# Performance work log

Hardware: AMD Instinct MI355X
Metric: run time of the kernel (lower is better)

## Reference

```python
import jax, jax.numpy as jnp
import numpy as np

B, S, D, H = 16, 1024, 768, 12
HD = D // H  # head_dim = 64


def setup_inputs() -> dict:
    key = jax.random.key(0)
    k1, k2, k3 = jax.random.split(key, 3)
    x = jax.random.normal(k1, (B, S, D), dtype=jnp.float32)
    # torch Linear default init ~ U(-1/sqrt(in), 1/sqrt(in)); use small normal for stability
    W_qkv = jax.random.normal(k2, (D, 3 * D), dtype=jnp.float32) * 0.02
    b_qkv = jnp.zeros((3 * D,), dtype=jnp.float32)
    W_out = jax.random.normal(k3, (D, D), dtype=jnp.float32) * 0.02
    b_out = jnp.zeros((D,), dtype=jnp.float32)
    return {"x": x, "W_qkv": W_qkv, "b_qkv": b_qkv, "W_out": W_out, "b_out": b_out, "mode": 0}


def reference(x, W_qkv, b_qkv, W_out, b_out, mode):
    # x: [B, S, D]; mode is unused (dropout is identity in eval)
    b, s, d = x.shape
    qkv = x @ W_qkv + b_qkv                                   # [B, S, 3D]
    qkv = qkv.reshape(b, s, 3, H, HD).transpose(2, 0, 3, 1, 4)  # [3, B, H, S, HD]
    Q, K, V = qkv[0], qkv[1], qkv[2]
    # NOTE: original has NO softmax and NO 1/sqrt(d) scale — pure matmul chain
    scores = jnp.einsum("bhsd,bhtd->bhst", Q, K)              # [B, H, S, S]
    out = jnp.einsum("bhst,bhtd->bhsd", scores, V)            # [B, H, S, HD]
    out = out.transpose(0, 2, 1, 3).reshape(b, s, d)          # [B, S, D]
    return out @ W_out + b_out
```

## Files before the change

kernel.cpp:

```cpp
#include <hip/hip_runtime.h>
#include <hip/hip_bf16.h>


typedef __attribute__((ext_vector_type(8))) short bf16x8;
typedef __attribute__((ext_vector_type(4))) short short4v;
typedef __attribute__((ext_vector_type(4))) float f32x4;
typedef __attribute__((ext_vector_type(4))) float float4v;

typedef __attribute__((address_space(1))) const unsigned char ga_u8;
typedef __attribute__((address_space(3))) unsigned char la_u8;

__device__ __forceinline__ unsigned short f2bf(float f) {
  union { float f; unsigned int u; } v; v.f = f;
  unsigned int u = v.u;
  return (unsigned short)((u + 0x7FFFu + ((u >> 16) & 1u)) >> 16);
}

__global__ __launch_bounds__(256) void cvt_f32_bf16(const float* __restrict__ in,
                                                    unsigned short* __restrict__ out) {
  const long long i = (long long)(blockIdx.x * 256 + threadIdx.x) * 8;
  float4v v0 = *(const float4v*)(in + i);
  float4v v1 = *(const float4v*)(in + i + 4);
  bf16x8 o;
  o[0] = (short)f2bf(v0[0]); o[1] = (short)f2bf(v0[1]);
  o[2] = (short)f2bf(v0[2]); o[3] = (short)f2bf(v0[3]);
  o[4] = (short)f2bf(v1[0]); o[5] = (short)f2bf(v1[1]);
  o[6] = (short)f2bf(v1[2]); o[7] = (short)f2bf(v1[3]);
  *(bf16x8*)(out + i) = o;
}

__global__ __launch_bounds__(256) void transpose_cvt(const float* __restrict__ in,
                                                     unsigned short* __restrict__ out,
                                                     int R, int C) {
  __shared__ unsigned short tile[32][33];
  const int bx = blockIdx.x * 32;
  const int by = blockIdx.y * 32;
  const int tx = threadIdx.x & 31, ty = threadIdx.x >> 5;
  #pragma unroll
  for (int i = 0; i < 32; i += 8)
    tile[ty + i][tx] = f2bf(in[(long long)(by + ty + i) * C + bx + tx]);
  __syncthreads();
  #pragma unroll
  for (int i = 0; i < 32; i += 8)
    out[(long long)(bx + ty + i) * R + by + tx] = tile[tx][ty + i];
}

struct GemmArgs {
  const void* A;
  const unsigned short* BT;
  void* C;
  unsigned short* KT;
  unsigned short* VT;
  const float* bias;
  int K;
  int lda, ldbt, ldc;
  long long sA1, sB1, sC1;
};


#define MFMA_(a, b, c) __builtin_amdgcn_mfma_f32_16x16x32_bf16(a, b, c, 0, 0, 0)
#define TBV { asm volatile("s_waitcnt vmcnt(3)" ::: "memory");                 \
              __builtin_amdgcn_s_barrier(); asm volatile("" ::: "memory"); }

template <int OMODE>
__global__ __launch_bounds__(512, 1) void gemm1b(GemmArgs g) {
  __shared__ unsigned short L[69632];

  const int gx = gridDim.x, gy = gridDim.y;
  const int nwg = gx * gy * gridDim.z;
  int flat = (blockIdx.z * gy + blockIdx.y) * gx + blockIdx.x;
  flat = (flat & 7) * (nwg >> 3) + (flat >> 3);
  const int gxy = gx * gy;
  const int bz = flat / gxy;
  const int rem = flat - bz * gxy;
  const int by = rem / gx;
  const int bx = rem - by * gx;

  const long long offA = bz * g.sA1;
  const long long offB = bz * g.sB1;
  const long long offC = bz * g.sC1;
  const int bm = by * 256, bn = bx * 192;

  const int tid = threadIdx.x;
  const int lane = tid & 63, wave = tid >> 6;
  const int wm = wave >> 2, wn = wave & 3;
  const int l15 = lane & 15, l4 = lane >> 4;

  const int lof0 = l15 * 64 + (((l4 + l15) * 8) & 63);
  const int lof1 = l15 * 64 + ((32 + (l4 + l15) * 8) & 63);
  const int wmA = wm * 8192;
  const int wnB = wn * 3072;

  int LA[4], DA[4], LB[3], DB[3];
  #pragma unroll
  for (int r = 0; r < 4; ++r) {
    const int c = tid + r * 512;
    const int row = c >> 3, j = c & 7;
    LA[r] = row * g.lda + ((j - row) & 7) * 8;
    DA[r] = c * 8;
  }
  #pragma unroll
  for (int r = 0; r < 3; ++r) {
    const int c = tid + r * 512;
    const int row = c >> 3, j = c & 7;
    LB[r] = row * g.ldbt + ((j - row) & 7) * 8;
    DB[r] = c * 8;
  }

  const unsigned short* Ab = (const unsigned short*)g.A + offA + (long long)bm * g.lda;
  const unsigned short* Bb = g.BT + offB + (long long)bn * g.ldbt;

  auto stA = [&](int bufsel, const unsigned short* p) {
    unsigned short* dst = &L[bufsel * 16384];
    #pragma unroll
    for (int r = 0; r < 4; ++r)
      __builtin_amdgcn_global_load_lds((ga_u8*)(p + LA[r]), (la_u8*)(dst + DA[r]), 16, 0, 0);
  };
  auto stB = [&](int bb, const unsigned short* p) {
    unsigned short* dst = &L[32768 + bb * 12288];
    #pragma unroll
    for (int r = 0; r < 3; ++r)
      __builtin_amdgcn_global_load_lds((ga_u8*)(p + LB[r]), (la_u8*)(dst + DB[r]), 16, 0, 0);
  };

  const f32x4 fz = {0.f, 0.f, 0.f, 0.f};
  f32x4 acc[8][3];
  #pragma unroll
  for (int i = 0; i < 8; ++i)
    #pragma unroll
    for (int j = 0; j < 3; ++j) acc[i][j] = fz;

  const unsigned short* pA = Ab;
  const unsigned short* pB = Bb;

  stA(0, pA); pA += 64;
  stB(0, pB); pB += 64;
  stB(1, pB); pB += 64;
  TBV

  bf16x8 af0[8], bf0[3], af1[8], bf1[3];
#define RD_HALF(dstA, dstB, bc, br, LOF)                                       \
  {                                                                            \
    const unsigned short* As_ = &L[(bc) * 16384 + wmA];                        \
    const unsigned short* Bs_ = &L[32768 + (br) * 12288 + wnB];                \
    _Pragma("unroll")                                                          \
    for (int x = 0; x < 3; ++x) dstB[x] = *(const bf16x8*)&Bs_[x * 1024 + LOF];\
    _Pragma("unroll")                                                          \
    for (int x = 0; x < 8; ++x) dstA[x] = *(const bf16x8*)&As_[x * 1024 + LOF];\
  }

  int bufc = 0, bbr = 0, bbs = 2;
  RD_HALF(af0, bf0, 0, 0, lof0)

  const int NT = g.K >> 6;
  for (int t = 0; t < NT; ++t) {
    RD_HALF(af1, bf1, bufc, bbr, lof1)
    stA(bufc ^ 1, pA); pA += 64;
    stB(bbs, pB); pB += 64;

    __builtin_amdgcn_s_setprio(1);
    #pragma unroll
    for (int nf = 0; nf < 3; ++nf)
      #pragma unroll
      for (int rj = 0; rj < 8; ++rj)
        acc[rj][nf] = MFMA_(af0[rj], bf0[nf], acc[rj][nf]);
    #pragma unroll
    for (int nf = 0; nf < 3; ++nf)
      #pragma unroll
      for (int rj = 0; rj < 8; ++rj)
        acc[rj][nf] = MFMA_(af1[rj], bf1[nf], acc[rj][nf]);
    __builtin_amdgcn_s_setprio(0);

    TBV
    bufc ^= 1;
    bbr = (bbr == 2) ? 0 : bbr + 1;
    bbs = (bbs == 2) ? 0 : bbs + 1;
    RD_HALF(af0, bf0, bufc, bbr, lof0)
  }

  const int row0 = bm + wm * 128 + l4 * 4;
  const int col0 = wn * 48 + l15;
  if (OMODE == 2) {
    #pragma unroll
    for (int mf = 0; mf < 8; ++mf)
      #pragma unroll
      for (int nf = 0; nf < 3; ++nf) {
        const int col = bn + col0 + nf * 16;
        const float bv = g.bias[col];
        #pragma unroll
        for (int ii = 0; ii < 4; ++ii)
          ((float*)g.C)[offC + (long long)(row0 + mf * 16 + ii) * g.ldc + col] =
              acc[mf][nf][ii] + bv;
      }
  } else if (bn < 768) {
    #pragma unroll
    for (int mf = 0; mf < 8; ++mf)
      #pragma unroll
      for (int nf = 0; nf < 3; ++nf) {
        const int col = bn + col0 + nf * 16;
        const float bv = g.bias[col];
        #pragma unroll
        for (int ii = 0; ii < 4; ++ii)
          ((unsigned short*)g.C)[(long long)(row0 + mf * 16 + ii) * 768 + col] =
              f2bf(acc[mf][nf][ii] + bv);
      }
  } else {
    unsigned short* T = (bn < 1536) ? g.KT : g.VT;
    const int rbase = (bn < 1536) ? 768 : 1536;
    const int b = bm >> 10;
    const int t0 = (row0 & 1023);
    #pragma unroll
    for (int nf = 0; nf < 3; ++nf) {
      const int gcol = bn + col0 + nf * 16;
      const float bv = g.bias[gcol];
      const int cr = gcol - rbase;
      const int h = cr >> 6, d = cr & 63;
      unsigned short* Tb = T + ((long long)(b * 12 + h) * 64 + d) * 1024;
      #pragma unroll
      for (int mf = 0; mf < 8; ++mf) {
        short4v sv;
        #pragma unroll
        for (int ii = 0; ii < 4; ++ii) sv[ii] = (short)f2bf(acc[mf][nf][ii] + bv);
        *(short4v*)&Tb[t0 + mf * 16] = sv;
      }
    }
  }
}

__global__ __launch_bounds__(256) void ktv_mfma(const unsigned short* __restrict__ KT,
                                                const unsigned short* __restrict__ VT,
                                                unsigned short* __restrict__ Mh) {
  __shared__ unsigned short L[2][2][4096];
  const int z = blockIdx.x;
  const int tid = threadIdx.x;
  const int lane = tid & 63, wave = tid >> 6;
  const int l15 = lane & 15, l4 = lane >> 4;

  const int lof0 = l15 * 64 + (((l4 + l15) * 8) & 63);
  const int lof1 = l15 * 64 + ((32 + (l4 + l15) * 8) & 63);

  int LS[2], DS[2];
  #pragma unroll
  for (int r = 0; r < 2; ++r) {
    const int c = tid + r * 256;
    const int row = c >> 3, j = c & 7;
    LS[r] = row * 1024 + ((j - row) & 7) * 8;
    DS[r] = c * 8;
  }
  const unsigned short* Ab = KT + (long long)z * 65536;
  const unsigned short* Bb = VT + (long long)z * 65536;

  auto stg = [&](int buf, const unsigned short* pa, const unsigned short* pb) {
    #pragma unroll
    for (int r = 0; r < 2; ++r) {
      __builtin_amdgcn_global_load_lds((ga_u8*)(pa + LS[r]), (la_u8*)(&L[buf][0][0] + DS[r]), 16, 0, 0);
      __builtin_amdgcn_global_load_lds((ga_u8*)(pb + LS[r]), (la_u8*)(&L[buf][1][0] + DS[r]), 16, 0, 0);
    }
  };

  const f32x4 fz = {0.f, 0.f, 0.f, 0.f};
  f32x4 acc[4];
  #pragma unroll
  for (int i = 0; i < 4; ++i) acc[i] = fz;

  const int eb = wave * 1024;
  stg(0, Ab, Bb);
  for (int t = 0; t < 16; ++t) {
    asm volatile("s_waitcnt vmcnt(0)" ::: "memory");
    __builtin_amdgcn_s_barrier();
    asm volatile("" ::: "memory");
    const int buf = t & 1;
    bf16x8 bv0 = *(const bf16x8*)&L[buf][1][eb + lof0];
    bf16x8 bv1 = *(const bf16x8*)&L[buf][1][eb + lof1];
    bf16x8 a0[4], a1[4];
    #pragma unroll
    for (int mf = 0; mf < 4; ++mf) {
      a0[mf] = *(const bf16x8*)&L[buf][0][mf * 1024 + lof0];
      a1[mf] = *(const bf16x8*)&L[buf][0][mf * 1024 + lof1];
    }
    if (t < 15) stg(buf ^ 1, Ab + (t + 1) * 64, Bb + (t + 1) * 64);
    #pragma unroll
    for (int mf = 0; mf < 4; ++mf) acc[mf] = MFMA_(a0[mf], bv0, acc[mf]);
    #pragma unroll
    for (int mf = 0; mf < 4; ++mf) acc[mf] = MFMA_(a1[mf], bv1, acc[mf]);
    __builtin_amdgcn_s_barrier();
    asm volatile("" ::: "memory");
  }

  unsigned short* mb = Mh + (long long)z * 4096;
  const int e = wave * 16 + l15;
  #pragma unroll
  for (int mf = 0; mf < 4; ++mf)
    #pragma unroll
    for (int ii = 0; ii < 4; ++ii)
      mb[(mf * 16 + l4 * 4 + ii) * 64 + e] = f2bf(acc[mf][ii]);
}

__global__ __launch_bounds__(256) void gemm_w2t(const unsigned short* __restrict__ WoutT,
                                                const unsigned short* __restrict__ Mh,
                                                unsigned short* __restrict__ W2T) {
  constexpr int LDT = 72;
  __shared__ unsigned short As[128 * LDT];
  __shared__ unsigned short Bs[64 * LDT];

  const int bm = blockIdx.x * 128;
  const int z = blockIdx.y;
  const int b = z / 12, h = z % 12;
  const int tid = threadIdx.x;
  const int lane = tid & 63, wave = tid >> 6;
  const int l15 = lane & 15, l4 = lane >> 4;
  const int srow = tid >> 3, scg = (tid & 7) * 8;

  const unsigned short* Abase = WoutT + (long long)bm * 768 + h * 64;
  #pragma unroll
  for (int s = 0; s < 4; ++s) {
    const int row = s * 32 + srow;
    *(bf16x8*)&As[row * LDT + scg] =
        *(const bf16x8*)(Abase + (long long)row * 768 + scg);
  }
  #pragma unroll
  for (int s = 0; s < 2; ++s) {
    const int row = s * 32 + srow;
    *(bf16x8*)&Bs[row * LDT + scg] =
        *(const bf16x8*)(Mh + (long long)z * 4096 + row * 64 + scg);
  }
  __syncthreads();

  const f32x4 fz = {0.f, 0.f, 0.f, 0.f};
  f32x4 acc[2][4];
  #pragma unroll
  for (int i = 0; i < 2; ++i)
    #pragma unroll
    for (int j = 0; j < 4; ++j) acc[i][j] = fz;

  #pragma unroll
  for (int ks = 0; ks < 64; ks += 32) {
    const int kk = ks + l4 * 8;
    bf16x8 af[2], bfv[4];
    #pragma unroll
    for (int i = 0; i < 2; ++i)
      af[i] = *(const bf16x8*)&As[(wave * 32 + i * 16 + l15) * LDT + kk];
    #pragma unroll
    for (int i = 0; i < 4; ++i)
      bfv[i] = *(const bf16x8*)&Bs[(i * 16 + l15) * LDT + kk];
    #pragma unroll
    for (int mi = 0; mi < 2; ++mi)
      #pragma unroll
      for (int ni = 0; ni < 4; ++ni)
        acc[mi][ni] = MFMA_(af[mi], bfv[ni], acc[mi][ni]);
  }

  unsigned short* Cb = W2T + (long long)b * 589824 + h * 64;
  #pragma unroll
  for (int mi = 0; mi < 2; ++mi)
    #pragma unroll
    for (int ni = 0; ni < 4; ++ni)
      #pragma unroll
      for (int ii = 0; ii < 4; ++ii) {
        const int row = bm + wave * 32 + mi * 16 + l4 * 4 + ii;
        const int col = ni * 16 + l15;
        Cb[(long long)row * 768 + col] = f2bf(acc[mi][ni][ii]);
      }
}

extern "C" void kernel_launch(void* const* d_in, const int* in_sizes, int n_in,
                              void* d_out, int out_size, void* d_ws, size_t ws_size,
                              hipStream_t stream) {
  (void)in_sizes; (void)n_in; (void)out_size; (void)ws_size;
  const float* x    = (const float*)d_in[0];
  const float* Wqkv = (const float*)d_in[1];
  const float* bqkv = (const float*)d_in[2];
  const float* Wout = (const float*)d_in[3];
  const float* bout = (const float*)d_in[4];
  float* out = (float*)d_out;

  char* ws = (char*)d_ws;
  size_t off = 0;
  auto carve = [&](size_t bytes) {
    char* p = ws + off;
    off += (bytes + 255) & ~(size_t)255;
    return p;
  };
  unsigned short* WqkvT = (unsigned short*)carve((size_t)2304 * 768 * 2);
  unsigned short* WoutT = (unsigned short*)carve((size_t)768 * 768 * 2);
  unsigned short* Qbuf  = (unsigned short*)carve((size_t)16384 * 768 * 2);
  unsigned short* KT    = (unsigned short*)carve((size_t)192 * 64 * 1024 * 2);
  unsigned short* VT    = (unsigned short*)carve((size_t)192 * 64 * 1024 * 2);
  unsigned short* Mh    = (unsigned short*)carve((size_t)192 * 64 * 64 * 2);
  unsigned short* xbf   = (unsigned short*)carve((size_t)16384 * 768 * 2);
  unsigned short* W2T   = xbf;
  carve((size_t)1 << 18);

  cvt_f32_bf16<<<dim3(16384 * 768 / 8 / 256), 256, 0, stream>>>(x, xbf);
  transpose_cvt<<<dim3(2304 / 32, 768 / 32), 256, 0, stream>>>(Wqkv, WqkvT, 768, 2304);
  transpose_cvt<<<dim3(768 / 32, 768 / 32), 256, 0, stream>>>(Wout, WoutT, 768, 768);

  GemmArgs g1{};
  g1.A = xbf; g1.BT = WqkvT; g1.C = Qbuf; g1.KT = KT; g1.VT = VT; g1.bias = bqkv;
  g1.K = 768; g1.lda = 768; g1.ldbt = 768; g1.ldc = 768;
  gemm1b<1><<<dim3(12, 64, 1), 512, 0, stream>>>(g1);

  ktv_mfma<<<dim3(192), 256, 0, stream>>>(KT, VT, Mh);

  gemm_w2t<<<dim3(6, 192), 256, 0, stream>>>(WoutT, Mh, W2T);

  GemmArgs g3{};
  g3.A = Qbuf; g3.BT = W2T; g3.C = out; g3.bias = bout;
  g3.K = 768; g3.lda = 768; g3.ldbt = 768; g3.ldc = 768;
  g3.sA1 = 786432;
  g3.sB1 = 589824;
  g3.sC1 = 786432;
  gemm1b<2><<<dim3(4, 4, 16), 512, 0, stream>>>(g3);
}
```

Baseline: 133.6 us.

## Load B operand directly from global into registers, halve LDS for 2 blocks/CU

The GEMM kernel stops staging the B (transposed weight) tile through LDS. Each wave now loads its B fragments straight from global memory into registers and double-buffers them in two register sets. A still uses the LDS double buffer, and the main loop is unrolled by two to alternate buffers. With LDS cut to 64KB, launch bounds allow two workgroups per CU for more occupancy and latency hiding, at the cost of uncoalesced per-lane global B reads, higher register pressure, and a retuned vmcnt wait that must stay correct.

```diff
diff --git a/kernel.cpp b/kernel.cpp
--- a/kernel.cpp
+++ b/kernel.cpp
@@ -59,12 +59,38 @@
 
 
 #define MFMA_(a, b, c) __builtin_amdgcn_mfma_f32_16x16x32_bf16(a, b, c, 0, 0, 0)
-#define TBV { asm volatile("s_waitcnt vmcnt(3)" ::: "memory");                 \
+#define FENCE asm volatile("" ::: "memory");
+#define TBV { asm volatile("s_waitcnt vmcnt(6)" ::: "memory");                 \
               __builtin_amdgcn_s_barrier(); asm volatile("" ::: "memory"); }
 
+#define RD_A(dst, bc, LOF)                                                     \
+  {                                                                            \
+    const unsigned short* As_ = &L[(bc) * 16384 + wmA];                        \
+    _Pragma("unroll")                                                          \
+    for (int x = 0; x < 8; ++x) dst[x] = *(const bf16x8*)&As_[x * 1024 + LOF]; \
+  }
+
+#define BLOAD(dst, p)                                                          \
+  {                                                                            \
+    _Pragma("unroll")                                                          \
+    for (int nf = 0; nf < 3; ++nf) {                                           \
+      dst[nf][0] = *(const bf16x8*)((p) + nf * nfs);                           \
+      dst[nf][1] = *(const bf16x8*)((p) + nf * nfs + 32);                      \
+    }                                                                          \
+  }
+
+#define MFMA_HALF(afr, bsrc, kh)                                               \
+  {                                                                            \
+    _Pragma("unroll")                                                          \
+    for (int nf = 0; nf < 3; ++nf)                                             \
+      _Pragma("unroll")                                                        \
+      for (int rj = 0; rj < 8; ++rj)                                           \
+        acc[rj][nf] = MFMA_(afr[rj], bsrc[nf][kh], acc[rj][nf]);               \
+  }
+
 template <int OMODE>
-__global__ __launch_bounds__(512, 1) void gemm1b(GemmArgs g) {
-  __shared__ unsigned short L[69632];
+__global__ __launch_bounds__(512, 2) void gemm1b(GemmArgs g) {
+  __shared__ unsigned short L[32768];
 
   const int gx = gridDim.x, gy = gridDim.y;
   const int nwg = gx * gy * gridDim.z;
@@ -89,9 +115,8 @@
   const int lof0 = l15 * 64 + (((l4 + l15) * 8) & 63);
   const int lof1 = l15 * 64 + ((32 + (l4 + l15) * 8) & 63);
   const int wmA = wm * 8192;
-  const int wnB = wn * 3072;
-
-  int LA[4], DA[4], LB[3], DB[3];
+
+  int LA[4], DA[4];
   #pragma unroll
   for (int r = 0; r < 4; ++r) {
     const int c = tid + r * 512;
@@ -99,16 +124,8 @@
     LA[r] = row * g.lda + ((j - row) & 7) * 8;
     DA[r] = c * 8;
   }
-  #pragma unroll
-  for (int r = 0; r < 3; ++r) {
-    const int c = tid + r * 512;
-    const int row = c >> 3, j = c & 7;
-    LB[r] = row * g.ldbt + ((j - row) & 7) * 8;
-    DB[r] = c * 8;
-  }
 
   const unsigned short* Ab = (const unsigned short*)g.A + offA + (long long)bm * g.lda;
-  const unsigned short* Bb = g.BT + offB + (long long)bn * g.ldbt;
 
   auto stA = [&](int bufsel, const unsigned short* p) {
     unsigned short* dst = &L[bufsel * 16384];
@@ -116,12 +133,10 @@
     for (int r = 0; r < 4; ++r)
       __builtin_amdgcn_global_load_lds((ga_u8*)(p + LA[r]), (la_u8*)(dst + DA[r]), 16, 0, 0);
   };
-  auto stB = [&](int bb, const unsigned short* p) {
-    unsigned short* dst = &L[32768 + bb * 12288];
-    #pragma unroll
-    for (int r = 0; r < 3; ++r)
-      __builtin_amdgcn_global_load_lds((ga_u8*)(p + LB[r]), (la_u8*)(dst + DB[r]), 16, 0, 0);
-  };
+
+  const int nfs = 16 * g.ldbt;
+  const unsigned short* pBg =
+      g.BT + offB + (long long)(bn + wn * 48 + l15) * g.ldbt + l4 * 8;
 
   const f32x4 fz = {0.f, 0.f, 0.f, 0.f};
   f32x4 acc[8][3];
@@ -131,51 +146,36 @@
     for (int j = 0; j < 3; ++j) acc[i][j] = fz;
 
   const unsigned short* pA = Ab;
-  const unsigned short* pB = Bb;
+  bf16x8 af0[8], af1[8], bX[3][2], bY[3][2];
 
   stA(0, pA); pA += 64;
-  stB(0, pB); pB += 64;
-  stB(1, pB); pB += 64;
+  FENCE
+  BLOAD(bX, pBg); pBg += 64;
   TBV
-
-  bf16x8 af0[8], bf0[3], af1[8], bf1[3];
-#define RD_HALF(dstA, dstB, bc, br, LOF)                                       \
-  {                                                                            \
-    const unsigned short* As_ = &L[(bc) * 16384 + wmA];                        \
-    const unsigned short* Bs_ = &L[32768 + (br) * 12288 + wnB];                \
-    _Pragma("unroll")                                                          \
-    for (int x = 0; x < 3; ++x) dstB[x] = *(const bf16x8*)&Bs_[x * 1024 + LOF];\
-    _Pragma("unroll")                                                          \
-    for (int x = 0; x < 8; ++x) dstA[x] = *(const bf16x8*)&As_[x * 1024 + LOF];\
-  }
-
-  int bufc = 0, bbr = 0, bbs = 2;
-  RD_HALF(af0, bf0, 0, 0, lof0)
-
-  const int NT = g.K >> 6;
-  for (int t = 0; t < NT; ++t) {
-    RD_HALF(af1, bf1, bufc, bbr, lof1)
-    stA(bufc ^ 1, pA); pA += 64;
-    stB(bbs, pB); pB += 64;
-
+  RD_A(af0, 0, lof0)
+
+  const int NP = g.K >> 7;
+  for (int i = 0; i < NP; ++i) {
+    RD_A(af1, 0, lof1)
+    stA(1, pA); pA += 64;
+    FENCE
+    BLOAD(bY, pBg); pBg += 64;
     __builtin_amdgcn_s_setprio(1);
-    #pragma unroll
-    for (int nf = 0; nf < 3; ++nf)
-      #pragma unroll
-      for (int rj = 0; rj < 8; ++rj)
-        acc[rj][nf] = MFMA_(af0[rj], bf0[nf], acc[rj][nf]);
-    #pragma unroll
-    for (int nf = 0; nf < 3; ++nf)
-      #pragma unroll
-      for (int rj = 0; rj < 8; ++rj)
-        acc[rj][nf] = MFMA_(af1[rj], bf1[nf], acc[rj][nf]);
+    MFMA_HALF(af0, bX, 0)
+    MFMA_HALF(af1, bX, 1)
     __builtin_amdgcn_s_setprio(0);
-
     TBV
-    bufc ^= 1;
-    bbr = (bbr == 2) ? 0 : bbr + 1;
-    bbs = (bbs == 2) ? 0 : bbs + 1;
-    RD_HALF(af0, bf0, bufc, bbr, lof0)
+    RD_A(af0, 1, lof0)
+    RD_A(af1, 1, lof1)
+    stA(0, pA); pA += 64;
+    FENCE
+    BLOAD(bX, pBg); pBg += 64;
+    __builtin_amdgcn_s_setprio(1);
+    MFMA_HALF(af0, bY, 0)
+    MFMA_HALF(af1, bY, 1)
+    __builtin_amdgcn_s_setprio(0);
+    TBV
+    RD_A(af0, 0, lof0)
   }
 
   const int row0 = bm + wm * 128 + l4 * 4;
```

After: 172.3 us. 1.29x slower.
